# Kernel optimization log

Hardware: AMD Instinct MI355X
Metric: run time of the kernel (lower is better)

The kernel has to match this reference:

```python
import jax, jax.numpy as jnp
import numpy as np

B, L, D = 4096, 50, 64
U, V, R = 100000, 100000, 5

def _lin(key, fan_out, fan_in):
    kw, kb = jax.random.split(key)
    s = 1.0 / np.sqrt(fan_in)
    return (jax.random.uniform(kw, (fan_out, fan_in), jnp.float32, -s, s),
            jax.random.uniform(kb, (fan_out,), jnp.float32, -s, s))

def setup_inputs() -> dict:
    key = jax.random.key(0)
    ks = jax.random.split(key, 12)
    w_r1_w, w_r1_b = _lin(ks[0], D, 2 * D)
    w_r2_w, w_r2_b = _lin(ks[1], D, D)
    att1_w, att1_b = _lin(ks[2], D, 2 * D)
    att2_w, att2_b = _lin(ks[3], D, D)
    att3_w, att3_b = _lin(ks[4], 1, D)
    return {
        "nodes": jax.random.randint(ks[5], (B,), 0, U),
        "history_uv": jax.random.randint(ks[6], (B, L), 0, V),
        "history_r": jax.random.randint(ks[7], (B, L), 0, R),
        "history_uvt": jax.random.randint(ks[8], (B, L), 0, 512),
        "v2e_w": jax.random.normal(ks[9], (V, D), jnp.float32) * 0.05,
        "u2e_w": jax.random.normal(ks[10], (U, D), jnp.float32) * 0.05,
        "r2e_w": jax.random.normal(ks[11], (R, D), jnp.float32) * 0.05,
        "w_r1_w": w_r1_w, "w_r1_b": w_r1_b,
        "w_r2_w": w_r2_w, "w_r2_b": w_r2_b,
        "att1_w": att1_w, "att1_b": att1_b,
        "att2_w": att2_w, "att2_b": att2_b,
        "att3_w": att3_w, "att3_b": att3_b,
    }

def reference(nodes, history_uv, history_r, history_uvt,
              v2e_w, u2e_w, r2e_w,
              w_r1_w, w_r1_b, w_r2_w, w_r2_b,
              att1_w, att1_b, att2_w, att2_b, att3_w, att3_b):
    # Gathers (uv=True branch): item embeddings for neighbor history, user rep for node
    e_uv = v2e_w[history_uv]          # (B, L, D)
    e_r = r2e_w[history_r]            # (B, L, D)
    uv_rep = u2e_w[nodes]             # (B, D)
    # Two-layer MLP on [e_uv ; e_r]
    x = jnp.concatenate([e_uv, e_r], axis=-1)               # (B, L, 2D)
    h = jax.nn.relu(jnp.einsum('blk,dk->bld', x, w_r1_w) + w_r1_b)
    o = jax.nn.relu(jnp.einsum('blk,dk->bld', h, w_r2_w) + w_r2_b)  # (B, L, D)
    # GraphRec Attention: MLP([o ; uv_rep]) -> scalar -> softmax over neighbors
    uv_b = jnp.broadcast_to(uv_rep[:, None, :], o.shape)     # (B, L, D)
    xa = jnp.concatenate([o, uv_b], axis=-1)                 # (B, L, 2D)
    a = jax.nn.relu(jnp.einsum('blk,dk->bld', xa, att1_w) + att1_b)
    a = jax.nn.relu(jnp.einsum('blk,dk->bld', a, att2_w) + att2_b)
    s = jnp.einsum('bld,od->blo', a, att3_w)[..., 0] + att3_b[0]    # (B, L)
    w = jax.nn.softmax(s, axis=1)                            # softmax over neighbors
    # att_history = o^T @ att_w  per node
    out = jnp.einsum('bld,bl->bd', o, w)                     # (B, D)
    return out
```

## Files before the change

### kernel.cpp

```cpp
#include <hip/hip_runtime.h>


#define LNB 50

typedef _Float16 f16x8 __attribute__((ext_vector_type(8)));
typedef float    f32x4 __attribute__((ext_vector_type(4)));

struct __align__(16) SMem {
  _Float16 h[64 * 64];
  _Float16 o[64 * 64];
  int   iu[64];
  int   ir[64];
  float sc[64];
  float wt[64];
};

__device__ __forceinline__ int swz(int r, int bytecol) {
  return (r * 128 + bytecol) ^ ((r & 7) << 4);
}

__device__ __forceinline__ f16x8 cvt8(const float* __restrict__ p) {
  const float4 lo = *(const float4*)p;
  const float4 hi = *(const float4*)(p + 4);
  f16x8 a;
  a[0] = (_Float16)lo.x; a[1] = (_Float16)lo.y;
  a[2] = (_Float16)lo.z; a[3] = (_Float16)lo.w;
  a[4] = (_Float16)hi.x; a[5] = (_Float16)hi.y;
  a[6] = (_Float16)hi.z; a[7] = (_Float16)hi.w;
  return a;
}

__global__ void prep_weights(const float* __restrict__ w1, const float* __restrict__ w2,
                             const float* __restrict__ a1, const float* __restrict__ a2,
                             _Float16* __restrict__ wf) {
  int i = blockIdx.x * 256 + threadIdx.x;
  if (i < 8192) wf[i]         = (_Float16)w1[i];
  if (i < 4096) wf[8192 + i]  = (_Float16)w2[i];
  if (i < 8192) wf[12288 + i] = (_Float16)a1[i];
  if (i < 4096) wf[20480 + i] = (_Float16)a2[i];
}

__global__ __launch_bounds__(64, 2) void uvagg_kernel(
    const int* __restrict__ nodes,
    const int* __restrict__ hist_uv,
    const int* __restrict__ hist_r,
    const float* __restrict__ v2e,
    const float* __restrict__ u2e,
    const float* __restrict__ r2e,
    const float* __restrict__ b1,
    const float* __restrict__ b2,
    const float* __restrict__ ab1,
    const float* __restrict__ ab2,
    const float* __restrict__ a3w,
    const _Float16* __restrict__ wf,
    float* __restrict__ out) {
  __shared__ SMem W;
  const int lane = threadIdx.x;
  const int b = blockIdx.x;
  const int lr = lane & 15;
  const int kq = lane >> 4;

  if (lane < LNB) {
    W.iu[lane] = hist_uv[b * LNB + lane];
    W.ir[lane] = hist_r[b * LNB + lane];
  } else {
    W.iu[lane] = 0;
    W.ir[lane] = 0;
  }
  const int node = nodes[b];
  __syncthreads();

  const _Float16* w1f = wf;
  const _Float16* w2f = wf + 8192;
  const _Float16* a1f = wf + 12288;
  const _Float16* a2f = wf + 20480;

  {
    f16x8 Bf[4][4];
#pragma unroll
    for (int kt = 0; kt < 4; ++kt)
#pragma unroll
      for (int nt = 0; nt < 4; ++nt)
        Bf[kt][nt] = *(const f16x8*)(w1f + (nt * 16 + lr) * 128 + kt * 32 + kq * 8);

#pragma unroll
    for (int m = 0; m < 4; ++m) {
      const int r = m * 16 + lr;
      f16x8 A[4];
      if (r < LNB) {
        const float* pu = v2e + (size_t)W.iu[r] * 64;
        const float* pr = r2e + (size_t)W.ir[r] * 64;
        A[0] = cvt8(pu + kq * 8);
        A[1] = cvt8(pu + 32 + kq * 8);
        A[2] = cvt8(pr + kq * 8);
        A[3] = cvt8(pr + 32 + kq * 8);
      } else {
#pragma unroll
        for (int kt = 0; kt < 4; ++kt)
#pragma unroll
          for (int i = 0; i < 8; ++i) A[kt][i] = (_Float16)0.f;
      }
#pragma unroll
      for (int nt = 0; nt < 4; ++nt) {
        f32x4 acc = {0.f, 0.f, 0.f, 0.f};
#pragma unroll
        for (int kt = 0; kt < 4; ++kt)
          acc = __builtin_amdgcn_mfma_f32_16x16x32_f16(A[kt], Bf[kt][nt], acc, 0, 0, 0);
        const int c = nt * 16 + lr;
        const float bias = b1[c];
#pragma unroll
        for (int j = 0; j < 4; ++j) {
          const int row = m * 16 + kq * 4 + j;
          const float v = fmaxf(acc[j] + bias, 0.f);
          *(_Float16*)((char*)W.h + swz(row, 2 * c)) = (_Float16)v;
        }
      }
    }
  }
  __syncthreads();

  {
    f16x8 Bf[2][4];
#pragma unroll
    for (int kt = 0; kt < 2; ++kt)
#pragma unroll
      for (int nt = 0; nt < 4; ++nt)
        Bf[kt][nt] = *(const f16x8*)(w2f + (nt * 16 + lr) * 64 + kt * 32 + kq * 8);

#pragma unroll
    for (int m = 0; m < 4; ++m) {
      const int r = m * 16 + lr;
      f16x8 A0 = *(const f16x8*)((char*)W.h + swz(r, 2 * (kq * 8)));
      f16x8 A1v = *(const f16x8*)((char*)W.h + swz(r, 2 * (32 + kq * 8)));
#pragma unroll
      for (int nt = 0; nt < 4; ++nt) {
        f32x4 acc = {0.f, 0.f, 0.f, 0.f};
        acc = __builtin_amdgcn_mfma_f32_16x16x32_f16(A0, Bf[0][nt], acc, 0, 0, 0);
        acc = __builtin_amdgcn_mfma_f32_16x16x32_f16(A1v, Bf[1][nt], acc, 0, 0, 0);
        const int c = nt * 16 + lr;
        const float bias = b2[c];
#pragma unroll
        for (int j = 0; j < 4; ++j) {
          const int row = m * 16 + kq * 4 + j;
          const float v = fmaxf(acc[j] + bias, 0.f);
          *(_Float16*)((char*)W.o + swz(row, 2 * c)) = (_Float16)v;
        }
      }
    }
  }
  __syncthreads();

  {
    f16x8 Bf[4][4];
#pragma unroll
    for (int kt = 0; kt < 4; ++kt)
#pragma unroll
      for (int nt = 0; nt < 4; ++nt)
        Bf[kt][nt] = *(const f16x8*)(a1f + (nt * 16 + lr) * 128 + kt * 32 + kq * 8);

    const f16x8 U2 = cvt8(u2e + (size_t)node * 64 + kq * 8);
    const f16x8 U3 = cvt8(u2e + (size_t)node * 64 + 32 + kq * 8);

#pragma unroll
    for (int m = 0; m < 4; ++m) {
      const int r = m * 16 + lr;
      f16x8 A0 = *(const f16x8*)((char*)W.o + swz(r, 2 * (kq * 8)));
      f16x8 A1v = *(const f16x8*)((char*)W.o + swz(r, 2 * (32 + kq * 8)));
#pragma unroll
      for (int nt = 0; nt < 4; ++nt) {
        f32x4 acc = {0.f, 0.f, 0.f, 0.f};
        acc = __builtin_amdgcn_mfma_f32_16x16x32_f16(A0, Bf[0][nt], acc, 0, 0, 0);
        acc = __builtin_amdgcn_mfma_f32_16x16x32_f16(A1v, Bf[1][nt], acc, 0, 0, 0);
        acc = __builtin_amdgcn_mfma_f32_16x16x32_f16(U2, Bf[2][nt], acc, 0, 0, 0);
        acc = __builtin_amdgcn_mfma_f32_16x16x32_f16(U3, Bf[3][nt], acc, 0, 0, 0);
        const int c = nt * 16 + lr;
        const float bias = ab1[c];
#pragma unroll
        for (int j = 0; j < 4; ++j) {
          const int row = m * 16 + kq * 4 + j;
          const float v = fmaxf(acc[j] + bias, 0.f);
          *(_Float16*)((char*)W.h + swz(row, 2 * c)) = (_Float16)v;
        }
      }
    }
  }
  __syncthreads();

  {
    f16x8 Bf[2][4];
#pragma unroll
    for (int kt = 0; kt < 2; ++kt)
#pragma unroll
      for (int nt = 0; nt < 4; ++nt)
        Bf[kt][nt] = *(const f16x8*)(a2f + (nt * 16 + lr) * 64 + kt * 32 + kq * 8);

#pragma unroll
    for (int m = 0; m < 4; ++m) {
      const int r = m * 16 + lr;
      f16x8 A0 = *(const f16x8*)((char*)W.h + swz(r, 2 * (kq * 8)));
      f16x8 A1v = *(const f16x8*)((char*)W.h + swz(r, 2 * (32 + kq * 8)));
      float part[4] = {0.f, 0.f, 0.f, 0.f};
#pragma unroll
      for (int nt = 0; nt < 4; ++nt) {
        f32x4 acc = {0.f, 0.f, 0.f, 0.f};
        acc = __builtin_amdgcn_mfma_f32_16x16x32_f16(A0, Bf[0][nt], acc, 0, 0, 0);
        acc = __builtin_amdgcn_mfma_f32_16x16x32_f16(A1v, Bf[1][nt], acc, 0, 0, 0);
        const int c = nt * 16 + lr;
        const float bias = ab2[c];
        const float a3c = a3w[c];
#pragma unroll
        for (int j = 0; j < 4; ++j) {
          const float v = fmaxf(acc[j] + bias, 0.f);
          part[j] += v * a3c;
        }
      }
#pragma unroll
      for (int mask = 1; mask < 16; mask <<= 1)
#pragma unroll
        for (int j = 0; j < 4; ++j) part[j] += __shfl_xor(part[j], mask);
      if (lr == 0) {
#pragma unroll
        for (int j = 0; j < 4; ++j) W.sc[m * 16 + kq * 4 + j] = part[j];
      }
    }
  }
  __syncthreads();

  {
    float sv = (lane < LNB) ? W.sc[lane] : -1e30f;
    float mx = sv;
#pragma unroll
    for (int mask = 1; mask < 64; mask <<= 1) mx = fmaxf(mx, __shfl_xor(mx, mask));
    const float e = __expf(sv - mx);
    float s = e;
#pragma unroll
    for (int mask = 1; mask < 64; mask <<= 1) s += __shfl_xor(s, mask);
    W.wt[lane] = e / s;
  }
  __syncthreads();

  {
    float acc = 0.f;
    for (int l = 0; l < LNB; ++l) {
      const float wl = W.wt[l];
      const float ov = (float)(*(const _Float16*)((const char*)W.o + swz(l, 2 * lane)));
      acc += wl * ov;
    }
    out[(size_t)b * 64 + lane] = acc;
  }
}

extern "C" void kernel_launch(void* const* d_in, const int* in_sizes, int n_in,
                              void* d_out, int out_size, void* d_ws, size_t ws_size,
                              hipStream_t stream) {
  (void)in_sizes; (void)n_in; (void)out_size; (void)ws_size;
  const int* nodes = (const int*)d_in[0];
  const int* huv   = (const int*)d_in[1];
  const int* hr    = (const int*)d_in[2];
  const float* v2e = (const float*)d_in[4];
  const float* u2e = (const float*)d_in[5];
  const float* r2e = (const float*)d_in[6];
  const float* w1  = (const float*)d_in[7];
  const float* b1  = (const float*)d_in[8];
  const float* w2  = (const float*)d_in[9];
  const float* b2  = (const float*)d_in[10];
  const float* a1  = (const float*)d_in[11];
  const float* ab1 = (const float*)d_in[12];
  const float* a2  = (const float*)d_in[13];
  const float* ab2 = (const float*)d_in[14];
  const float* a3  = (const float*)d_in[15];

  _Float16* wf = (_Float16*)d_ws;
  prep_weights<<<32, 256, 0, stream>>>(w1, w2, a1, a2, wf);
  uvagg_kernel<<<4096, 64, 0, stream>>>(nodes, huv, hr, v2e, u2e, r2e,
                                        b1, b2, ab1, ab2, a3, wf,
                                        (float*)d_out);
}
```

Baseline: 157.1 us.

## Split fused kernel into dense per-row MLP kernel and attention kernel

Splits the single per-node kernel into two launches. The first runs the two-layer rating MLP over the flattened B*L rows in dense 64-row tiles, so the 14 padding rows per node are no longer computed, and writes the fp16 result to workspace. The second reads those rows back for the attention MLP, softmax and weighted sum. This removes wasted MFMA work and halves shared memory per block so more blocks can be resident, at the cost of an extra launch and a global write and read of the intermediate (about 26 MB in fp16).

```diff
diff --git a/kernel.cpp b/kernel.cpp
--- a/kernel.cpp
+++ b/kernel.cpp
@@ -5,15 +5,6 @@
 
 typedef _Float16 f16x8 __attribute__((ext_vector_type(8)));
 typedef float    f32x4 __attribute__((ext_vector_type(4)));
-
-struct __align__(16) SMem {
-  _Float16 h[64 * 64];
-  _Float16 o[64 * 64];
-  int   iu[64];
-  int   ir[64];
-  float sc[64];
-  float wt[64];
-};
 
 __device__ __forceinline__ int swz(int r, int bytecol) {
   return (r * 128 + bytecol) ^ ((r & 7) << 4);
@@ -40,40 +31,138 @@
   if (i < 4096) wf[20480 + i] = (_Float16)a2[i];
 }
 
-__global__ __launch_bounds__(64, 2) void uvagg_kernel(
-    const int* __restrict__ nodes,
+__global__ __launch_bounds__(64, 4) void mlp_kernel(
     const int* __restrict__ hist_uv,
     const int* __restrict__ hist_r,
     const float* __restrict__ v2e,
-    const float* __restrict__ u2e,
     const float* __restrict__ r2e,
     const float* __restrict__ b1,
     const float* __restrict__ b2,
+    const _Float16* __restrict__ wf,
+    _Float16* __restrict__ ows) {
+  __shared__ _Float16 T[64 * 64];
+  const int lane = threadIdx.x;
+  const int lr = lane & 15;
+  const int kq = lane >> 4;
+  const int r0 = blockIdx.x * 64;
+
+  const _Float16* w1f = wf;
+  const _Float16* w2f = wf + 8192;
+
+  {
+    f16x8 Bf[4][4];
+#pragma unroll
+    for (int kt = 0; kt < 4; ++kt)
+#pragma unroll
+      for (int nt = 0; nt < 4; ++nt)
+        Bf[kt][nt] = *(const f16x8*)(w1f + (nt * 16 + lr) * 128 + kt * 32 + kq * 8);
+
+    float bias1[4];
+#pragma unroll
+    for (int nt = 0; nt < 4; ++nt) bias1[nt] = b1[nt * 16 + lr];
+
+#pragma unroll
+    for (int m = 0; m < 4; ++m) {
+      const int r = r0 + m * 16 + lr;
+      const int iu = hist_uv[r];
+      const int ir = hist_r[r];
+      const float* pu = v2e + (size_t)iu * 64;
+      const float* pr = r2e + (size_t)ir * 64;
+      f16x8 A[4];
+      A[0] = cvt8(pu + kq * 8);
+      A[1] = cvt8(pu + 32 + kq * 8);
+      A[2] = cvt8(pr + kq * 8);
+      A[3] = cvt8(pr + 32 + kq * 8);
+#pragma unroll
+      for (int nt = 0; nt < 4; ++nt) {
+        f32x4 acc = {0.f, 0.f, 0.f, 0.f};
+#pragma unroll
+        for (int kt = 0; kt < 4; ++kt)
+          acc = __builtin_amdgcn_mfma_f32_16x16x32_f16(A[kt], Bf[kt][nt], acc, 0, 0, 0);
+        const int c = nt * 16 + lr;
+#pragma unroll
+        for (int j = 0; j < 4; ++j) {
+          const int row = m * 16 + kq * 4 + j;
+          const float v = fmaxf(acc[j] + bias1[nt], 0.f);
+          *(_Float16*)((char*)T + swz(row, 2 * c)) = (_Float16)v;
+        }
+      }
+    }
+  }
+  __syncthreads();
+
+  {
+    f16x8 Bf[2][4];
+#pragma unroll
+    for (int kt = 0; kt < 2; ++kt)
+#pragma unroll
+      for (int nt = 0; nt < 4; ++nt)
+        Bf[kt][nt] = *(const f16x8*)(w2f + (nt * 16 + lr) * 64 + kt * 32 + kq * 8);
+
+    float bias2[4];
+#pragma unroll
+    for (int nt = 0; nt < 4; ++nt) bias2[nt] = b2[nt * 16 + lr];
+
+#pragma unroll
+    for (int m = 0; m < 4; ++m) {
+      const int r = m * 16 + lr;
+      f16x8 A0  = *(const f16x8*)((char*)T + swz(r, 2 * (kq * 8)));
+      f16x8 A1v = *(const f16x8*)((char*)T + swz(r, 2 * (32 + kq * 8)));
+      f32x4 accs[4];
+#pragma unroll
+      for (int nt = 0; nt < 4; ++nt) {
+        f32x4 acc = {0.f, 0.f, 0.f, 0.f};
+        acc = __builtin_amdgcn_mfma_f32_16x16x32_f16(A0,  Bf[0][nt], acc, 0, 0, 0);
+        acc = __builtin_amdgcn_mfma_f32_16x16x32_f16(A1v, Bf[1][nt], acc, 0, 0, 0);
+        accs[nt] = acc;
+      }
+      asm volatile("s_waitcnt lgkmcnt(0)" ::: "memory");
+#pragma unroll
+      for (int nt = 0; nt < 4; ++nt) {
+        const int c = nt * 16 + lr;
+#pragma unroll
+        for (int j = 0; j < 4; ++j) {
+          const int row = m * 16 + kq * 4 + j;
+          const float v = fmaxf(accs[nt][j] + bias2[nt], 0.f);
+          *(_Float16*)((char*)T + swz(row, 2 * c)) = (_Float16)v;
+        }
+      }
+    }
+  }
+  __syncthreads();
+
+  {
+    char* dst = (char*)ows + (size_t)r0 * 128;
+#pragma unroll
+    for (int p = 0; p < 8; ++p) {
+      const int idx = p * 1024 + lane * 16;
+      f16x8 v = *(const f16x8*)((const char*)T + swz(idx >> 7, idx & 127));
+      *(f16x8*)(dst + idx) = v;
+    }
+  }
+}
+
+__global__ __launch_bounds__(64, 4) void att_kernel(
+    const int* __restrict__ nodes,
+    const float* __restrict__ u2e,
     const float* __restrict__ ab1,
     const float* __restrict__ ab2,
     const float* __restrict__ a3w,
     const _Float16* __restrict__ wf,
+    const _Float16* __restrict__ ows,
     float* __restrict__ out) {
-  __shared__ SMem W;
+  __shared__ _Float16 T[64 * 64];
+  __shared__ float sc[64];
+  __shared__ float wt[64];
   const int lane = threadIdx.x;
-  const int b = blockIdx.x;
   const int lr = lane & 15;
   const int kq = lane >> 4;
-
-  if (lane < LNB) {
-    W.iu[lane] = hist_uv[b * LNB + lane];
-    W.ir[lane] = hist_r[b * LNB + lane];
-  } else {
-    W.iu[lane] = 0;
-    W.ir[lane] = 0;
-  }
+  const int b = blockIdx.x;
   const int node = nodes[b];
-  __syncthreads();
-
-  const _Float16* w1f = wf;
-  const _Float16* w2f = wf + 8192;
+
   const _Float16* a1f = wf + 12288;
   const _Float16* a2f = wf + 20480;
+  const _Float16* ob = ows + (size_t)b * LNB * 64;
 
   {
     f16x8 Bf[4][4];
@@ -81,38 +170,40 @@
     for (int kt = 0; kt < 4; ++kt)
 #pragma unroll
       for (int nt = 0; nt < 4; ++nt)
-        Bf[kt][nt] = *(const f16x8*)(w1f + (nt * 16 + lr) * 128 + kt * 32 + kq * 8);
+        Bf[kt][nt] = *(const f16x8*)(a1f + (nt * 16 + lr) * 128 + kt * 32 + kq * 8);
+
+    const f16x8 U2 = cvt8(u2e + (size_t)node * 64 + kq * 8);
+    const f16x8 U3 = cvt8(u2e + (size_t)node * 64 + 32 + kq * 8);
+
+    float biasa1[4];
+#pragma unroll
+    for (int nt = 0; nt < 4; ++nt) biasa1[nt] = ab1[nt * 16 + lr];
 
 #pragma unroll
     for (int m = 0; m < 4; ++m) {
       const int r = m * 16 + lr;
-      f16x8 A[4];
+      f16x8 A0, A1v;
       if (r < LNB) {
-        const float* pu = v2e + (size_t)W.iu[r] * 64;
-        const float* pr = r2e + (size_t)W.ir[r] * 64;
-        A[0] = cvt8(pu + kq * 8);
-        A[1] = cvt8(pu + 32 + kq * 8);
-        A[2] = cvt8(pr + kq * 8);
-        A[3] = cvt8(pr + 32 + kq * 8);
+        const _Float16* orow = ob + (size_t)r * 64;
+        A0  = *(const f16x8*)(orow + kq * 8);
+        A1v = *(const f16x8*)(orow + 32 + kq * 8);
       } else {
 #pragma unroll
-        for (int kt = 0; kt < 4; ++kt)
-#pragma unroll
-          for (int i = 0; i < 8; ++i) A[kt][i] = (_Float16)0.f;
+        for (int i = 0; i < 8; ++i) { A0[i] = (_Float16)0.f; A1v[i] = (_Float16)0.f; }
       }
 #pragma unroll
       for (int nt = 0; nt < 4; ++nt) {
         f32x4 acc = {0.f, 0.f, 0.f, 0.f};
-#pragma unroll
-        for (int kt = 0; kt < 4; ++kt)
-          acc = __builtin_amdgcn_mfma_f32_16x16x32_f16(A[kt], Bf[kt][nt], acc, 0, 0, 0);
+        acc = __builtin_amdgcn_mfma_f32_16x16x32_f16(A0,  Bf[0][nt], acc, 0, 0, 0);
+        acc = __builtin_amdgcn_mfma_f32_16x16x32_f16(A1v, Bf[1][nt], acc, 0, 0, 0);
+        acc = __builtin_amdgcn_mfma_f32_16x16x32_f16(U2,  Bf[2][nt], acc, 0, 0, 0);
+        acc = __builtin_amdgcn_mfma_f32_16x16x32_f16(U3,  Bf[3][nt], acc, 0, 0, 0);
         const int c = nt * 16 + lr;
-        const float bias = b1[c];
 #pragma unroll
         for (int j = 0; j < 4; ++j) {
           const int row = m * 16 + kq * 4 + j;
-          const float v = fmaxf(acc[j] + bias, 0.f);
-          *(_Float16*)((char*)W.h + swz(row, 2 * c)) = (_Float16)v;
+          const float v = fmaxf(acc[j] + biasa1[nt], 0.f);
+          *(_Float16*)((char*)T + swz(row, 2 * c)) = (_Float16)v;
         }
       }
     }
@@ -125,93 +216,30 @@
     for (int kt = 0; kt < 2; ++kt)
 #pragma unroll
       for (int nt = 0; nt < 4; ++nt)
-        Bf[kt][nt] = *(const f16x8*)(w2f + (nt * 16 + lr) * 64 + kt * 32 + kq * 8);
+        Bf[kt][nt] = *(const f16x8*)(a2f + (nt * 16 + lr) * 64 + kt * 32 + kq * 8);
+
+    float biasa2[4], a3c[4];
+#pragma unroll
+    for (int nt = 0; nt < 4; ++nt) {
+      biasa2[nt] = ab2[nt * 16 + lr];
+      a3c[nt] = a3w[nt * 16 + lr];
+    }
 
 #pragma unroll
     for (int m = 0; m < 4; ++m) {
       const int r = m * 16 + lr;
-      f16x8 A0 = *(const f16x8*)((char*)W.h + swz(r, 2 * (kq * 8)));
-      f16x8 A1v = *(const f16x8*)((char*)W.h + swz(r, 2 * (32 + kq * 8)));
+      f16x8 A0  = *(const f16x8*)((char*)T + swz(r, 2 * (kq * 8)));
+      f16x8 A1v = *(const f16x8*)((char*)T + swz(r, 2 * (32 + kq * 8)));
+      float part[4] = {0.f, 0.f, 0.f, 0.f};
 #pragma unroll
       for (int nt = 0; nt < 4; ++nt) {
         f32x4 acc = {0.f, 0.f, 0.f, 0.f};
-        acc = __builtin_amdgcn_mfma_f32_16x16x32_f16(A0, Bf[0][nt], acc, 0, 0, 0);
+        acc = __builtin_amdgcn_mfma_f32_16x16x32_f16(A0,  Bf[0][nt], acc, 0, 0, 0);
         acc = __builtin_amdgcn_mfma_f32_16x16x32_f16(A1v, Bf[1][nt], acc, 0, 0, 0);
-        const int c = nt * 16 + lr;
-        const float bias = b2[c];
 #pragma unroll
         for (int j = 0; j < 4; ++j) {
-          const int row = m * 16 + kq * 4 + j;
-          const float v = fmaxf(acc[j] + bias, 0.f);
-          *(_Float16*)((char*)W.o + swz(row, 2 * c)) = (_Float16)v;
-        }
-      }
-    }
-  }
-  __syncthreads();
-
-  {
-    f16x8 Bf[4][4];
-#pragma unroll
-    for (int kt = 0; kt < 4; ++kt)
-#pragma unroll
-      for (int nt = 0; nt < 4; ++nt)
-        Bf[kt][nt] = *(const f16x8*)(a1f + (nt * 16 + lr) * 128 + kt * 32 + kq * 8);
-
-    const f16x8 U2 = cvt8(u2e + (size_t)node * 64 + kq * 8);
-    const f16x8 U3 = cvt8(u2e + (size_t)node * 64 + 32 + kq * 8);
-
-#pragma unroll
-    for (int m = 0; m < 4; ++m) {
-      const int r = m * 16 + lr;
-      f16x8 A0 = *(const f16x8*)((char*)W.o + swz(r, 2 * (kq * 8)));
-      f16x8 A1v = *(const f16x8*)((char*)W.o + swz(r, 2 * (32 + kq * 8)));
-#pragma unroll
-      for (int nt = 0; nt < 4; ++nt) {
-        f32x4 acc = {0.f, 0.f, 0.f, 0.f};
-        acc = __builtin_amdgcn_mfma_f32_16x16x32_f16(A0, Bf[0][nt], acc, 0, 0, 0);
-        acc = __builtin_amdgcn_mfma_f32_16x16x32_f16(A1v, Bf[1][nt], acc, 0, 0, 0);
-        acc = __builtin_amdgcn_mfma_f32_16x16x32_f16(U2, Bf[2][nt], acc, 0, 0, 0);
-        acc = __builtin_amdgcn_mfma_f32_16x16x32_f16(U3, Bf[3][nt], acc, 0, 0, 0);
-        const int c = nt * 16 + lr;
-        const float bias = ab1[c];
-#pragma unroll
-        for (int j = 0; j < 4; ++j) {
-          const int row = m * 16 + kq * 4 + j;
-          const float v = fmaxf(acc[j] + bias, 0.f);
-          *(_Float16*)((char*)W.h + swz(row, 2 * c)) = (_Float16)v;
-        }
-      }
-    }
-  }
-  __syncthreads();
-
-  {
-    f16x8 Bf[2][4];
-#pragma unroll
-    for (int kt = 0; kt < 2; ++kt)
-#pragma unroll
-      for (int nt = 0; nt < 4; ++nt)
-        Bf[kt][nt] = *(const f16x8*)(a2f + (nt * 16 + lr) * 64 + kt * 32 + kq * 8);
-
-#pragma unroll
-    for (int m = 0; m < 4; ++m) {
-      const int r = m * 16 + lr;
-      f16x8 A0 = *(const f16x8*)((char*)W.h + swz(r, 2 * (kq * 8)));
-      f16x8 A1v = *(const f16x8*)((char*)W.h + swz(r, 2 * (32 + kq * 8)));
-      float part[4] = {0.f, 0.f, 0.f, 0.f};
-#pragma unroll
-      for (int nt = 0; nt < 4; ++nt) {
-        f32x4 acc = {0.f, 0.f, 0.f, 0.f};
-        acc = __builtin_amdgcn_mfma_f32_16x16x32_f16(A0, Bf[0][nt], acc, 0, 0, 0);
-        acc = __builtin_amdgcn_mfma_f32_16x16x32_f16(A1v, Bf[1][nt], acc, 0, 0, 0);
-        const int c = nt * 16 + lr;
-        const float bias = ab2[c];
-        const float a3c = a3w[c];
-#pragma unroll
-        for (int j = 0; j < 4; ++j) {
-          const float v = fmaxf(acc[j] + bias, 0.f);
-          part[j] += v * a3c;
+          const float v = fmaxf(acc[j] + biasa2[nt], 0.f);
+          part[j] += v * a3c[nt];
         }
       }
 #pragma unroll
@@ -220,14 +248,14 @@
         for (int j = 0; j < 4; ++j) part[j] += __shfl_xor(part[j], mask);
       if (lr == 0) {
 #pragma unroll
-        for (int j = 0; j < 4; ++j) W.sc[m * 16 + kq * 4 + j] = part[j];
-      }
-    }
-  }
-  __syncthreads();
-
-  {
-    float sv = (lane < LNB) ? W.sc[lane] : -1e30f;
+        for (int j = 0; j < 4; ++j) sc[m * 16 + kq * 4 + j] = part[j];
+      }
+    }
+  }
+  __syncthreads();
+
+  {
+    float sv = (lane < LNB) ? sc[lane] : -1e30f;
     float mx = sv;
 #pragma unroll
     for (int mask = 1; mask < 64; mask <<= 1) mx = fmaxf(mx, __shfl_xor(mx, mask));
@@ -235,17 +263,15 @@
     float s = e;
 #pragma unroll
     for (int mask = 1; mask < 64; mask <<= 1) s += __shfl_xor(s, mask);
-    W.wt[lane] = e / s;
+    wt[lane] = e / s;
   }
   __syncthreads();
 
   {
     float acc = 0.f;
-    for (int l = 0; l < LNB; ++l) {
-      const float wl = W.wt[l];
-      const float ov = (float)(*(const _Float16*)((const char*)W.o + swz(l, 2 * lane)));
-      acc += wl * ov;
-    }
+    const _Float16* oc = ob + lane;
+#pragma unroll
+    for (int l = 0; l < LNB; ++l) acc += wt[l] * (float)oc[(size_t)l * 64];
     out[(size_t)b * 64 + lane] = acc;
   }
 }
@@ -270,9 +296,11 @@
   const float* ab2 = (const float*)d_in[14];
   const float* a3  = (const float*)d_in[15];
 
-  _Float16* wf = (_Float16*)d_ws;
+  _Float16* wf  = (_Float16*)d_ws;
+  _Float16* ows = (_Float16*)((char*)d_ws + 65536);
+
   prep_weights<<<32, 256, 0, stream>>>(w1, w2, a1, a2, wf);
-  uvagg_kernel<<<4096, 64, 0, stream>>>(nodes, huv, hr, v2e, u2e, r2e,
-                                        b1, b2, ab1, ab2, a3, wf,
-                                        (float*)d_out);
-}
+  mlp_kernel<<<3200, 64, 0, stream>>>(huv, hr, v2e, r2e, b1, b2, wf, ows);
+  att_kernel<<<4096, 64, 0, stream>>>(nodes, u2e, ab1, ab2, a3, wf, ows,
+                                      (float*)d_out);
+}
```

Measured after the change: 162.3 us. 3.3% more time.
